# Optimization experiments

Measured on AMD Instinct MI355X. Metric: run time of the kernel, lower is better.

Reference implementation:

```python
import jax, jax.numpy as jnp
import numpy as np

T = 0.07          # temperature (params[1])
B, N, D, C = 128, 100000, 128, 40  # batch, bank size (outputSize=K), feat dim (inputSize-1), n classes
STDV = 1.0 / np.sqrt((D + 1) / 3.0)  # init scale from __init__


def setup_inputs() -> dict:
    key = jax.random.key(0)
    k1, k2, k3, k4, k5, k6 = jax.random.split(key, 6)
    x = jax.random.normal(k1, (B, D), dtype=jnp.float32)
    x = x / jnp.linalg.norm(x, axis=1, keepdims=True)  # unit-norm features (keeps exp(out/T) in range)
    y = jax.random.randint(k2, (B,), 0, N)
    labels = jax.random.randint(k3, (B,), 0, C)
    bank_labels = jax.random.randint(k4, (N,), 0, C).astype(jnp.float32)
    mem_feats = (jax.random.uniform(k5, (N, D), dtype=jnp.float32) * 2.0 - 1.0) * STDV
    da_feats = (jax.random.uniform(k6, (N, D), dtype=jnp.float32) * 2.0 - 1.0) * STDV
    memory = jnp.concatenate([bank_labels[:, None], mem_feats], axis=1)      # [N, 1+D], col 0 = label
    memory_da = jnp.concatenate([bank_labels[:, None], da_feats], axis=1)    # [N, 1+D], col 0 = label
    return {"x": x, "y": y, "labels": labels, "memory_da": memory_da, "memory": memory}


def reference(x, y, labels, memory_da, memory):
    # NCEFunction.forward: out[b,n] = exp(x[b] . memory_da[n,1:] / T), Z-normalized per row (Z<0 branch)
    n_out = memory_da.shape[0]
    feats = memory_da[:, 1:]                               # [N, D] gathered features
    out = jnp.exp(jnp.einsum('bd,nd->bn', x, feats) / T)   # [B, N] (torch bmm over repeated bank)
    Z1 = out.mean(axis=1, keepdims=True) * n_out           # per-row Z estimate
    out = out / Z1
    # idx: per-label torch.where loop -> expressed densely as a boolean match matrix [B, N]
    idx_mask = memory_da[None, :, 0] == labels[:, None].astype(memory_da.dtype)
    return out, idx_mask
```

## Files before the change

### kernel.cpp

```cpp
#include <hip/hip_runtime.h>
#include <hip/hip_bf16.h>

#define NB 128
#define NMEM 100000
#define ND 128
constexpr float K2 = 20.6099442241331655f;

constexpr int LROW = ND + 8;
constexpr int NTP = NMEM / 32;
constexpr int GRID = 512;
constexpr int NWAVES = GRID * 4;
constexpr int ZSTRIDE = 16;

typedef __attribute__((ext_vector_type(8))) __bf16 bf16x8;
typedef __attribute__((ext_vector_type(4))) float f32x4;
struct bf4 { __bf16 a, b, c, d; };

template<bool PASS2>
__global__ __launch_bounds__(256, 2) void nce_wave(
    const float* __restrict__ x,
    const int* __restrict__ labels,
    const float* __restrict__ mem_da,
    float* __restrict__ zbuf,
    float* __restrict__ out,
    float* __restrict__ maskout)
{
  __shared__ __bf16 xs[NB * LROW];
  __shared__ float aux[NB];
  __shared__ float zl[NB];

  const int tid = threadIdx.x;

  const float4* x4 = (const float4*)x;
  float4 xv[16];
  #pragma unroll
  for (int i = 0; i < 16; ++i) xv[i] = x4[tid + i * 256];
  #pragma unroll
  for (int i = 0; i < 16; ++i) {
    int g4 = tid + i * 256;
    *(bf4*)&xs[(g4 >> 5) * LROW + (g4 & 31) * 4] =
        bf4{(__bf16)xv[i].x, (__bf16)xv[i].y, (__bf16)xv[i].z, (__bf16)xv[i].w};
  }
  if (tid < NB) {
    if (PASS2) aux[tid] = -__log2f(zbuf[tid * ZSTRIDE]);
    else { aux[tid] = (float)labels[tid]; zl[tid] = 0.f; }
  }
  __syncthreads();

  const int wid = tid >> 6, lane = tid & 63, q = lane >> 4, l16 = lane & 15;
  const int wgid = blockIdx.x * 4 + wid;

  float lblb[8];
  #pragma unroll
  for (int mt = 0; mt < 8; ++mt) lblb[mt] = aux[mt * 16 + l16];

  float zacc[8];
  #pragma unroll
  for (int mt = 0; mt < 8; ++mt) zacc[mt] = 0.f;

  for (int t = wgid; t < NTP; t += NWAVES) {
    f32x4 acc[2][8];
    float ln[2];

    #pragma unroll
    for (int h = 0; h < 2; ++h) {
      const int n0 = t * 32 + h * 16;
      const float* rowp = mem_da + (size_t)(n0 + l16) * 129;
      if (!PASS2) ln[h] = rowp[0];

      bf16x8 ab[4];
      #pragma unroll
      for (int kc = 0; kc < 4; ++kc) {
        float tmp[8];
        __builtin_memcpy(tmp, rowp + 1 + kc * 32 + q * 8, 32);
        #pragma unroll
        for (int j = 0; j < 8; ++j) ab[kc][j] = (__bf16)tmp[j];
      }

      #pragma unroll
      for (int mt = 0; mt < 8; ++mt) acc[h][mt] = (f32x4){0.f, 0.f, 0.f, 0.f};
      #pragma unroll
      for (int kc = 0; kc < 4; ++kc) {
        const int ko = kc * 32 + q * 8;
        #pragma unroll
        for (int mt = 0; mt < 8; ++mt) {
          bf16x8 xb = *(const bf16x8*)&xs[(mt * 16 + l16) * LROW + ko];
          acc[h][mt] = __builtin_amdgcn_mfma_f32_16x16x32_bf16(ab[kc], xb, acc[h][mt], 0, 0, 0);
        }
      }
    }

    float ml[2][4];
    if (!PASS2) {
      #pragma unroll
      for (int h = 0; h < 2; ++h)
        #pragma unroll
        for (int r = 0; r < 4; ++r) ml[h][r] = __shfl(ln[h], q * 4 + r, 16);
    }

    #pragma unroll
    for (int mt = 0; mt < 8; ++mt) {
      const size_t base = (size_t)(mt * 16 + l16) * NMEM + t * 32 + q * 4;
      if (!PASS2) {
        f32x4 mk0, mk1;
        float zs = 0.f;
        #pragma unroll
        for (int r = 0; r < 4; ++r) {
          zs += exp2f(acc[0][mt][r] * K2);
          zs += exp2f(acc[1][mt][r] * K2);
          mk0[r] = (ml[0][r] == lblb[mt]) ? 1.0f : 0.0f;
          mk1[r] = (ml[1][r] == lblb[mt]) ? 1.0f : 0.0f;
        }
        zacc[mt] += zs;
        __builtin_nontemporal_store(mk0, (f32x4*)&maskout[base]);
        __builtin_nontemporal_store(mk1, (f32x4*)&maskout[base + 16]);
      } else {
        f32x4 ov0, ov1;
        #pragma unroll
        for (int r = 0; r < 4; ++r) {
          ov0[r] = exp2f(__builtin_fmaf(acc[0][mt][r], K2, lblb[mt]));
          ov1[r] = exp2f(__builtin_fmaf(acc[1][mt][r], K2, lblb[mt]));
        }
        __builtin_nontemporal_store(ov0, (f32x4*)&out[base]);
        __builtin_nontemporal_store(ov1, (f32x4*)&out[base + 16]);
      }
    }
  }

  if (!PASS2) {
    #pragma unroll
    for (int mt = 0; mt < 8; ++mt) {
      float v = zacc[mt];
      v += __shfl_xor(v, 16);
      v += __shfl_xor(v, 32);
      if (lane < 16) atomicAdd(&zl[mt * 16 + lane], v);
    }
    __syncthreads();
    if (tid < NB) atomicAdd(&zbuf[tid * ZSTRIDE], zl[tid]);
  }
}

extern "C" void kernel_launch(void* const* d_in, const int* in_sizes, int n_in,
                              void* d_out, int out_size, void* d_ws, size_t ws_size,
                              hipStream_t stream) {
  const float* x      = (const float*)d_in[0];
  const int* labels   = (const int*)d_in[2];
  const float* mem_da = (const float*)d_in[3];
  float* out     = (float*)d_out;
  float* maskout = out + (size_t)NB * NMEM;
  float* zbuf    = (float*)d_ws;

  hipMemsetAsync(zbuf, 0, NB * ZSTRIDE * sizeof(float), stream);
  nce_wave<false><<<GRID, 256, 0, stream>>>(x, labels, mem_da, zbuf, nullptr, maskout);
  nce_wave<true ><<<GRID, 256, 0, stream>>>(x, labels, mem_da, zbuf, out, nullptr);
}
```

Before: 216.9 us.

## Interleave MFMA with epilogue per M-tile and enlarge grid to one pass over tiles

Loads both halves of the bank tile into bf16 registers first, then computes each M-tile's accumulators and immediately runs its exp and store epilogue. This avoids keeping all 16 accumulator vectors live at once. The x staging is split into chunks of four loads to lower peak register use. The grid grows so each wave handles about one tile, intended to raise parallelism and let stores overlap with MFMA work, at the cost of repeating the x-to-shared staging in more blocks.

```diff
diff --git a/kernel.cpp b/kernel.cpp
--- a/kernel.cpp
+++ b/kernel.cpp
@@ -8,7 +8,7 @@
 
 constexpr int LROW = ND + 8;
 constexpr int NTP = NMEM / 32;
-constexpr int GRID = 512;
+constexpr int GRID = 782;
 constexpr int NWAVES = GRID * 4;
 constexpr int ZSTRIDE = 16;
 
@@ -32,14 +32,17 @@
   const int tid = threadIdx.x;
 
   const float4* x4 = (const float4*)x;
-  float4 xv[16];
   #pragma unroll
-  for (int i = 0; i < 16; ++i) xv[i] = x4[tid + i * 256];
-  #pragma unroll
-  for (int i = 0; i < 16; ++i) {
-    int g4 = tid + i * 256;
-    *(bf4*)&xs[(g4 >> 5) * LROW + (g4 & 31) * 4] =
-        bf4{(__bf16)xv[i].x, (__bf16)xv[i].y, (__bf16)xv[i].z, (__bf16)xv[i].w};
+  for (int c = 0; c < 4; ++c) {
+    float4 xv[4];
+    #pragma unroll
+    for (int i = 0; i < 4; ++i) xv[i] = x4[tid + (c * 4 + i) * 256];
+    #pragma unroll
+    for (int i = 0; i < 4; ++i) {
+      int g4 = tid + (c * 4 + i) * 256;
+      *(bf4*)&xs[(g4 >> 5) * LROW + (g4 & 31) * 4] =
+          bf4{(__bf16)xv[i].x, (__bf16)xv[i].y, (__bf16)xv[i].z, (__bf16)xv[i].w};
+    }
   }
   if (tid < NB) {
     if (PASS2) aux[tid] = -__log2f(zbuf[tid * ZSTRIDE]);
@@ -59,34 +62,18 @@
   for (int mt = 0; mt < 8; ++mt) zacc[mt] = 0.f;
 
   for (int t = wgid; t < NTP; t += NWAVES) {
-    f32x4 acc[2][8];
+    bf16x8 ab[2][4];
     float ln[2];
-
     #pragma unroll
     for (int h = 0; h < 2; ++h) {
-      const int n0 = t * 32 + h * 16;
-      const float* rowp = mem_da + (size_t)(n0 + l16) * 129;
+      const float* rowp = mem_da + (size_t)(t * 32 + h * 16 + l16) * 129;
       if (!PASS2) ln[h] = rowp[0];
-
-      bf16x8 ab[4];
       #pragma unroll
       for (int kc = 0; kc < 4; ++kc) {
         float tmp[8];
         __builtin_memcpy(tmp, rowp + 1 + kc * 32 + q * 8, 32);
         #pragma unroll
-        for (int j = 0; j < 8; ++j) ab[kc][j] = (__bf16)tmp[j];
-      }
-
-      #pragma unroll
-      for (int mt = 0; mt < 8; ++mt) acc[h][mt] = (f32x4){0.f, 0.f, 0.f, 0.f};
-      #pragma unroll
-      for (int kc = 0; kc < 4; ++kc) {
-        const int ko = kc * 32 + q * 8;
-        #pragma unroll
-        for (int mt = 0; mt < 8; ++mt) {
-          bf16x8 xb = *(const bf16x8*)&xs[(mt * 16 + l16) * LROW + ko];
-          acc[h][mt] = __builtin_amdgcn_mfma_f32_16x16x32_bf16(ab[kc], xb, acc[h][mt], 0, 0, 0);
-        }
+        for (int j = 0; j < 8; ++j) ab[h][kc][j] = (__bf16)tmp[j];
       }
     }
 
@@ -100,14 +87,22 @@
 
     #pragma unroll
     for (int mt = 0; mt < 8; ++mt) {
+      f32x4 a0 = (f32x4){0.f, 0.f, 0.f, 0.f};
+      f32x4 a1 = (f32x4){0.f, 0.f, 0.f, 0.f};
+      #pragma unroll
+      for (int kc = 0; kc < 4; ++kc) {
+        bf16x8 xb = *(const bf16x8*)&xs[(mt * 16 + l16) * LROW + kc * 32 + q * 8];
+        a0 = __builtin_amdgcn_mfma_f32_16x16x32_bf16(ab[0][kc], xb, a0, 0, 0, 0);
+        a1 = __builtin_amdgcn_mfma_f32_16x16x32_bf16(ab[1][kc], xb, a1, 0, 0, 0);
+      }
       const size_t base = (size_t)(mt * 16 + l16) * NMEM + t * 32 + q * 4;
       if (!PASS2) {
         f32x4 mk0, mk1;
         float zs = 0.f;
         #pragma unroll
         for (int r = 0; r < 4; ++r) {
-          zs += exp2f(acc[0][mt][r] * K2);
-          zs += exp2f(acc[1][mt][r] * K2);
+          zs += exp2f(a0[r] * K2);
+          zs += exp2f(a1[r] * K2);
           mk0[r] = (ml[0][r] == lblb[mt]) ? 1.0f : 0.0f;
           mk1[r] = (ml[1][r] == lblb[mt]) ? 1.0f : 0.0f;
         }
@@ -118,8 +113,8 @@
         f32x4 ov0, ov1;
         #pragma unroll
         for (int r = 0; r < 4; ++r) {
-          ov0[r] = exp2f(__builtin_fmaf(acc[0][mt][r], K2, lblb[mt]));
-          ov1[r] = exp2f(__builtin_fmaf(acc[1][mt][r], K2, lblb[mt]));
+          ov0[r] = exp2f(__builtin_fmaf(a0[r], K2, lblb[mt]));
+          ov1[r] = exp2f(__builtin_fmaf(a1[r], K2, lblb[mt]));
         }
         __builtin_nontemporal_store(ov0, (f32x4*)&out[base]);
         __builtin_nontemporal_store(ov1, (f32x4*)&out[base + 16]);
```

Result: slower. 240.6 us (+10.9%).

## Store unnormalized exp once and rescale in a separate elementwise pass

Applied to the files above, without the earlier changes.

Drops the second GEMM pass, which recomputed the bank dot products to apply the normalizer. The first kernel now writes both the unnormalized exponentials and the mask while accumulating Z. A new elementwise kernel then multiplies each row by 1/Z in place. This trades the repeated matmul and bank read for an extra full read and write of the output matrix; the main grid is also doubled.

```diff
diff --git a/kernel.cpp b/kernel.cpp
--- a/kernel.cpp
+++ b/kernel.cpp
@@ -8,23 +8,25 @@
 
 constexpr int LROW = ND + 8;
 constexpr int NTP = NMEM / 32;
-constexpr int GRID = 512;
+constexpr int GRID = 1024;
 constexpr int NWAVES = GRID * 4;
 constexpr int ZSTRIDE = 16;
+constexpr int RGRID = 2048;
 
 typedef __attribute__((ext_vector_type(8))) __bf16 bf16x8;
 typedef __attribute__((ext_vector_type(4))) float f32x4;
 struct bf4 { __bf16 a, b, c, d; };
 
-template<bool PASS2>
-__global__ __launch_bounds__(256, 2) void nce_wave(
+__global__ __launch_bounds__(256, 2) void nce_pass1(
     const float* __restrict__ x,
     const int* __restrict__ labels,
     const float* __restrict__ mem_da,
     float* __restrict__ zbuf,
-    float* __restrict__ out,
+    float* __restrict__ expout,
     float* __restrict__ maskout)
 {
+  if (blockIdx.x * 4 >= NTP) return;
+
   __shared__ __bf16 xs[NB * LROW];
   __shared__ float aux[NB];
   __shared__ float zl[NB];
@@ -32,19 +34,19 @@
   const int tid = threadIdx.x;
 
   const float4* x4 = (const float4*)x;
-  float4 xv[16];
   #pragma unroll
-  for (int i = 0; i < 16; ++i) xv[i] = x4[tid + i * 256];
-  #pragma unroll
-  for (int i = 0; i < 16; ++i) {
-    int g4 = tid + i * 256;
-    *(bf4*)&xs[(g4 >> 5) * LROW + (g4 & 31) * 4] =
-        bf4{(__bf16)xv[i].x, (__bf16)xv[i].y, (__bf16)xv[i].z, (__bf16)xv[i].w};
+  for (int c = 0; c < 4; ++c) {
+    float4 xv[4];
+    #pragma unroll
+    for (int i = 0; i < 4; ++i) xv[i] = x4[tid + (c * 4 + i) * 256];
+    #pragma unroll
+    for (int i = 0; i < 4; ++i) {
+      int g4 = tid + (c * 4 + i) * 256;
+      *(bf4*)&xs[(g4 >> 5) * LROW + (g4 & 31) * 4] =
+          bf4{(__bf16)xv[i].x, (__bf16)xv[i].y, (__bf16)xv[i].z, (__bf16)xv[i].w};
+    }
   }
-  if (tid < NB) {
-    if (PASS2) aux[tid] = -__log2f(zbuf[tid * ZSTRIDE]);
-    else { aux[tid] = (float)labels[tid]; zl[tid] = 0.f; }
-  }
+  if (tid < NB) { aux[tid] = (float)labels[tid]; zl[tid] = 0.f; }
   __syncthreads();
 
   const int wid = tid >> 6, lane = tid & 63, q = lane >> 4, l16 = lane & 15;
@@ -64,9 +66,8 @@
 
     #pragma unroll
     for (int h = 0; h < 2; ++h) {
-      const int n0 = t * 32 + h * 16;
-      const float* rowp = mem_da + (size_t)(n0 + l16) * 129;
-      if (!PASS2) ln[h] = rowp[0];
+      const float* rowp = mem_da + (size_t)(t * 32 + h * 16 + l16) * 129;
+      ln[h] = rowp[0];
 
       bf16x8 ab[4];
       #pragma unroll
@@ -91,52 +92,58 @@
     }
 
     float ml[2][4];
-    if (!PASS2) {
+    #pragma unroll
+    for (int h = 0; h < 2; ++h)
       #pragma unroll
-      for (int h = 0; h < 2; ++h)
-        #pragma unroll
-        for (int r = 0; r < 4; ++r) ml[h][r] = __shfl(ln[h], q * 4 + r, 16);
-    }
+      for (int r = 0; r < 4; ++r) ml[h][r] = __shfl(ln[h], q * 4 + r, 16);
 
     #pragma unroll
     for (int mt = 0; mt < 8; ++mt) {
       const size_t base = (size_t)(mt * 16 + l16) * NMEM + t * 32 + q * 4;
-      if (!PASS2) {
-        f32x4 mk0, mk1;
-        float zs = 0.f;
-        #pragma unroll
-        for (int r = 0; r < 4; ++r) {
-          zs += exp2f(acc[0][mt][r] * K2);
-          zs += exp2f(acc[1][mt][r] * K2);
-          mk0[r] = (ml[0][r] == lblb[mt]) ? 1.0f : 0.0f;
-          mk1[r] = (ml[1][r] == lblb[mt]) ? 1.0f : 0.0f;
-        }
-        zacc[mt] += zs;
-        __builtin_nontemporal_store(mk0, (f32x4*)&maskout[base]);
-        __builtin_nontemporal_store(mk1, (f32x4*)&maskout[base + 16]);
-      } else {
-        f32x4 ov0, ov1;
-        #pragma unroll
-        for (int r = 0; r < 4; ++r) {
-          ov0[r] = exp2f(__builtin_fmaf(acc[0][mt][r], K2, lblb[mt]));
-          ov1[r] = exp2f(__builtin_fmaf(acc[1][mt][r], K2, lblb[mt]));
-        }
-        __builtin_nontemporal_store(ov0, (f32x4*)&out[base]);
-        __builtin_nontemporal_store(ov1, (f32x4*)&out[base + 16]);
+      f32x4 mk0, mk1, e0, e1;
+      float zs = 0.f;
+      #pragma unroll
+      for (int r = 0; r < 4; ++r) {
+        e0[r] = exp2f(acc[0][mt][r] * K2);
+        e1[r] = exp2f(acc[1][mt][r] * K2);
+        zs += e0[r] + e1[r];
+        mk0[r] = (ml[0][r] == lblb[mt]) ? 1.0f : 0.0f;
+        mk1[r] = (ml[1][r] == lblb[mt]) ? 1.0f : 0.0f;
       }
+      zacc[mt] += zs;
+      __builtin_nontemporal_store(mk0, (f32x4*)&maskout[base]);
+      __builtin_nontemporal_store(mk1, (f32x4*)&maskout[base + 16]);
+      __builtin_nontemporal_store(e0, (f32x4*)&expout[base]);
+      __builtin_nontemporal_store(e1, (f32x4*)&expout[base + 16]);
     }
   }
 
-  if (!PASS2) {
-    #pragma unroll
-    for (int mt = 0; mt < 8; ++mt) {
-      float v = zacc[mt];
-      v += __shfl_xor(v, 16);
-      v += __shfl_xor(v, 32);
-      if (lane < 16) atomicAdd(&zl[mt * 16 + lane], v);
-    }
-    __syncthreads();
-    if (tid < NB) atomicAdd(&zbuf[tid * ZSTRIDE], zl[tid]);
+  #pragma unroll
+  for (int mt = 0; mt < 8; ++mt) {
+    float v = zacc[mt];
+    v += __shfl_xor(v, 16);
+    v += __shfl_xor(v, 32);
+    if (lane < 16) atomicAdd(&zl[mt * 16 + lane], v);
+  }
+  __syncthreads();
+  if (tid < NB) atomicAdd(&zbuf[tid * ZSTRIDE], zl[tid]);
+}
+
+__global__ __launch_bounds__(256) void rescale(
+    float* __restrict__ out, const float* __restrict__ zbuf)
+{
+  __shared__ float sinv[NB];
+  if (threadIdx.x < NB) sinv[threadIdx.x] = 1.0f / zbuf[threadIdx.x * ZSTRIDE];
+  __syncthreads();
+
+  constexpr int TOT4 = NB * NMEM / 4;
+  constexpr int ROW4 = NMEM / 4;
+  const int stride = RGRID * 256;
+  for (int i = blockIdx.x * 256 + threadIdx.x; i < TOT4; i += stride) {
+    const float s = sinv[i / ROW4];
+    f32x4 v = __builtin_nontemporal_load((const f32x4*)out + i);
+    v[0] *= s; v[1] *= s; v[2] *= s; v[3] *= s;
+    __builtin_nontemporal_store(v, (f32x4*)out + i);
   }
 }
 
@@ -151,6 +158,6 @@
   float* zbuf    = (float*)d_ws;
 
   hipMemsetAsync(zbuf, 0, NB * ZSTRIDE * sizeof(float), stream);
-  nce_wave<false><<<GRID, 256, 0, stream>>>(x, labels, mem_da, zbuf, nullptr, maskout);
-  nce_wave<true ><<<GRID, 256, 0, stream>>>(x, labels, mem_da, zbuf, out, nullptr);
+  nce_pass1<<<GRID, 256, 0, stream>>>(x, labels, mem_da, zbuf, out, maskout);
+  rescale<<<RGRID, 256, 0, stream>>>(out, zbuf);
 }
```

Result: no change. 219.7 us (+1.3%).
